# Kernel optimization log

Measured on AMD Instinct MI355X. Metric: run time of the kernel, lower is better.

The kernel has to match this reference:

```python
import jax, jax.numpy as jnp
import numpy as np

VOCAB, EMBED = 50000, 256
MODULES, HEADS, HID = 2, 4, 64
B, S = 8, 2048
LABELS = 16


def setup_inputs() -> dict:
    key = jax.random.key(0)
    ks = jax.random.split(key, 12)
    seqs = jax.random.randint(ks[0], (B, S), 0, VOCAB)
    emb = jax.random.normal(ks[1], (VOCAB, EMBED), jnp.float32) * 0.02
    Wq = jax.random.normal(ks[2], (MODULES, HEADS, HID, EMBED), jnp.float32) * (1.0 / np.sqrt(EMBED))
    bq = jax.random.normal(ks[3], (MODULES, HEADS, HID), jnp.float32) * 0.01
    Wk = jax.random.normal(ks[4], (MODULES, HEADS, HID, EMBED), jnp.float32) * (1.0 / np.sqrt(EMBED))
    bk = jax.random.normal(ks[5], (MODULES, HEADS, HID), jnp.float32) * 0.01
    Wv = jax.random.normal(ks[6], (MODULES, HEADS, HID, EMBED), jnp.float32) * (1.0 / np.sqrt(EMBED))
    bv = jax.random.normal(ks[7], (MODULES, HEADS, HID), jnp.float32) * 0.01
    Wz = jax.random.normal(ks[8], (MODULES, EMBED, HEADS * HID), jnp.float32) * (1.0 / np.sqrt(HEADS * HID))
    bz = jax.random.normal(ks[9], (MODULES, EMBED), jnp.float32) * 0.01
    Wo = jax.random.normal(ks[10], (LABELS, S * EMBED), jnp.float32) * (1.0 / np.sqrt(S * EMBED))
    bo = jax.random.normal(ks[11], (LABELS,), jnp.float32) * 0.01
    return {"seqs": seqs, "emb": emb, "Wq": Wq, "bq": bq, "Wk": Wk, "bk": bk,
            "Wv": Wv, "bv": bv, "Wz": Wz, "bz": bz, "Wo": Wo, "bo": bo}


def _forward(seqs, emb, Wq, bq, Wk, bk, Wv, bv, Wz, bz, Wo, bo):
    x = emb[seqs]  # [B, S, E]
    scale = jnp.float32(EMBED) ** 0.5
    for m in range(MODULES):
        # per-head projections with relu (dropout=0 / eval mode)
        Q = jax.nn.relu(jnp.einsum('bse,hde->bhsd', x, Wq[m]) + bq[m][None, :, None, :])
        K = jax.nn.relu(jnp.einsum('bse,hde->bhsd', x, Wk[m]) + bk[m][None, :, None, :])
        V = jax.nn.relu(jnp.einsum('bse,hde->bhsd', x, Wv[m]) + bv[m][None, :, None, :])
        QK = jnp.einsum('bhsd,bhtd->bhst', Q, K) / scale  # [B,H,S,S]
        # double softmax: first over the query axis (torch dim=1 of [B,S,S]),
        # then over the key axis (torch dim=2)
        A = jax.nn.softmax(QK, axis=2)
        A = jax.nn.softmax(A, axis=3)
        Z = jnp.einsum('bhst,bhtd->bhsd', A, V)  # [B,H,S,HID]
        Zall = jnp.transpose(Z, (0, 2, 1, 3)).reshape(x.shape[0], S, HEADS * HID)
        ZF = jnp.einsum('bsk,ek->bse', Zall, Wz[m]) + bz[m]
        x = ZF + x  # residual (layer_norm=False)
    Xf = x.reshape(x.shape[0], S * EMBED)
    y = jax.nn.sigmoid(Xf @ Wo.T + bo)
    return y


def reference(seqs, emb, Wq, bq, Wk, bk, Wv, bv, Wz, bz, Wo, bo):
    return _forward(seqs, emb, Wq, bq, Wk, bk, Wv, bv, Wz, bz, Wo, bo)
```

## Files before the change

### kernel.cpp

```cpp
#include <hip/hip_runtime.h>
#include <math.h>

#define Bb 8
#define Ss 2048
#define Ee 256
#define Hh 4
#define Dd 64

typedef unsigned short u16;
typedef unsigned int u32;
typedef __attribute__((ext_vector_type(8))) short bf16x8;
typedef __attribute__((ext_vector_type(4))) float f32x4;

__device__ __forceinline__ u16 f2bf(float f) {
  union { float f; u32 u; } c; c.f = f;
  return (u16)((c.u + 0x7FFFu + ((c.u >> 16) & 1u)) >> 16);
}
__device__ __forceinline__ float bf2f(u16 u) {
  union { u32 u; float f; } c; c.u = ((u32)u) << 16;
  return c.f;
}
__device__ __forceinline__ float bf2fs(short s) { return bf2f((u16)s); }

__global__ __launch_bounds__(256) void k_w2b(const float* __restrict__ src,
                                             u16* __restrict__ dst) {
  int idx = (blockIdx.x * 256 + threadIdx.x) * 4;
  float4 v = *reinterpret_cast<const float4*>(src + idx);
  ushort4 o;
  o.x = f2bf(v.x); o.y = f2bf(v.y); o.z = f2bf(v.z); o.w = f2bf(v.w);
  *reinterpret_cast<ushort4*>(dst + idx) = o;
}

__global__ __launch_bounds__(256) void k_gather(const int* __restrict__ seqs,
                                                const float* __restrict__ emb,
                                                float* __restrict__ x,
                                                u16* __restrict__ xb) {
  int idx = blockIdx.x * 256 + threadIdx.x;
  int row = idx >> 6, c4 = idx & 63;
  int tok = seqs[row];
  float4 v = reinterpret_cast<const float4*>(emb)[(size_t)tok * 64 + c4];
  reinterpret_cast<float4*>(x)[(size_t)row * 64 + c4] = v;
  ushort4 o;
  o.x = f2bf(v.x); o.y = f2bf(v.y); o.z = f2bf(v.z); o.w = f2bf(v.w);
  reinterpret_cast<ushort4*>(xb)[(size_t)row * 64 + c4] = o;
}

__global__ __launch_bounds__(256) void k_qkvm(const u16* __restrict__ xb,
    const u16* __restrict__ Wqb, const u16* __restrict__ Wkb, const u16* __restrict__ Wvb,
    const float* __restrict__ bq, const float* __restrict__ bk, const float* __restrict__ bv,
    u16* __restrict__ Qf, u16* __restrict__ Kf, u16* __restrict__ Vf, int mod) {
  __shared__ short Xs[128][72];
  __shared__ short Ws[128][72];
  int tid = threadIdx.x;
  int bn = blockIdx.x;
  int arr = bn >> 1, coff = (bn & 1) << 7;
  const u16* W = (arr == 0 ? Wqb : arr == 1 ? Wkb : Wvb) + (size_t)mod * 256 * 256;
  const float* bias = (arr == 0 ? bq : arr == 1 ? bk : bv) + mod * 256;
  u16* Out = (arr == 0 ? Qf : arr == 1 ? Kf : Vf);
  float oscale = (arr == 0) ? 0.0625f : 1.0f;
  int s0 = blockIdx.y * 128;
  int lr = tid >> 1, lc = (tid & 1) << 5;
  int w = tid >> 6, lane = tid & 63, ml = lane & 15, q = lane >> 4;
  int sh = (w >> 1) << 6, th = (w & 1) << 6;
  f32x4 acc[4][4] = {};
  for (int k0 = 0; k0 < 256; k0 += 64) {
#pragma unroll
    for (int hh = 0; hh < 4; hh++) {
      *reinterpret_cast<bf16x8*>(&Xs[lr][lc + hh * 8]) =
          *reinterpret_cast<const bf16x8*>(xb + (size_t)(s0 + lr) * Ee + k0 + lc + hh * 8);
      *reinterpret_cast<bf16x8*>(&Ws[lr][lc + hh * 8]) =
          *reinterpret_cast<const bf16x8*>(W + (size_t)(coff + lr) * Ee + k0 + lc + hh * 8);
    }
    __syncthreads();
#pragma unroll
    for (int ks = 0; ks < 2; ks++) {
      bf16x8 af[4], bfr[4];
#pragma unroll
      for (int mt = 0; mt < 4; mt++)
        af[mt] = *reinterpret_cast<const bf16x8*>(&Xs[sh + mt * 16 + ml][ks * 32 + q * 8]);
#pragma unroll
      for (int nt = 0; nt < 4; nt++)
        bfr[nt] = *reinterpret_cast<const bf16x8*>(&Ws[th + nt * 16 + ml][ks * 32 + q * 8]);
#pragma unroll
      for (int mt = 0; mt < 4; mt++)
#pragma unroll
        for (int nt = 0; nt < 4; nt++)
          acc[mt][nt] = __builtin_amdgcn_mfma_f32_16x16x32_bf16(af[mt], bfr[nt], acc[mt][nt], 0, 0, 0);
    }
    __syncthreads();
  }
#pragma unroll
  for (int mt = 0; mt < 4; mt++)
#pragma unroll
    for (int nt = 0; nt < 4; nt++)
#pragma unroll
      for (int r = 0; r < 4; r++) {
        int gm = s0 + sh + mt * 16 + q * 4 + r;
        int cc = coff + th + nt * 16 + ml;
        float v = acc[mt][nt][r] + bias[cc];
        v = (v > 0.f ? v : 0.f) * oscale;
        Out[(size_t)gm * Ee + cc] = f2bf(v);
      }
}

__global__ __launch_bounds__(256) void k_vt(const u16* __restrict__ Vf,
                                            u16* __restrict__ Vt) {
  __shared__ u16 T[64][72];
  int tid = threadIdx.x;
  int t0 = blockIdx.x * 64;
  int z = blockIdx.y;
  int b = z >> 2, h = z & 3;
  int lr = tid >> 2, lc = (tid & 3) << 4;
#pragma unroll
  for (int hh = 0; hh < 2; hh++) {
    bf16x8 v = *reinterpret_cast<const bf16x8*>(
        Vf + (size_t)(b * Ss + t0 + lr) * Ee + h * Dd + lc + hh * 8);
#pragma unroll
    for (int j = 0; j < 8; j++) T[lr][lc + hh * 8 + j] = (u16)v[j];
  }
  __syncthreads();
#pragma unroll
  for (int j = 0; j < 16; j++) {
    Vt[((size_t)z * Dd + lr) * Ss + t0 + lc + j] = T[lc + j][lr];
  }
}

__global__ __launch_bounds__(256) void k_vsum(const u16* __restrict__ Vt,
                                              float* __restrict__ SV) {
  int z = blockIdx.y;
  int d = blockIdx.x * 4 + (threadIdx.x >> 6);
  int lane = threadIdx.x & 63;
  const u16* row = Vt + ((size_t)z * Dd + d) * Ss;
  float s = 0.f;
#pragma unroll
  for (int it = 0; it < 4; it++) {
    bf16x8 v = *reinterpret_cast<const bf16x8*>(row + it * 512 + lane * 8);
#pragma unroll
    for (int j = 0; j < 8; j++) s += bf2fs(v[j]);
  }
#pragma unroll
  for (int off = 32; off; off >>= 1) s += __shfl_xor(s, off);
  if (lane == 0) SV[(size_t)z * Dd + d] = s;
}

__global__ __launch_bounds__(256) void k_csum(const u16* __restrict__ Qf,
    const u16* __restrict__ Kf, float* __restrict__ llic) {
  __shared__ short Qs[2][128 * 72];
  __shared__ float csm[4][64];
  int tid = threadIdx.x;
  int z = blockIdx.y, b = z >> 2, h = z & 3;
  const u16* Qb = Qf + (size_t)b * Ss * Ee + h * Dd;
  const u16* Kb = Kf + (size_t)b * Ss * Ee + h * Dd;
  int t0 = blockIdx.x * 128;
  int lr = tid >> 1, lc = (tid & 1) << 5;
  int w = tid >> 6, lane = tid & 63, ml = lane & 15, q = lane >> 4;
  int sh = (w >> 1) << 6, th = (w & 1) << 6;
  bf16x8 kb[2][4];
#pragma unroll
  for (int ks = 0; ks < 2; ks++)
#pragma unroll
    for (int nt = 0; nt < 4; nt++)
      kb[ks][nt] = *reinterpret_cast<const bf16x8*>(
          Kb + (size_t)(t0 + th + nt * 16 + ml) * Ee + ks * 32 + q * 8);
  float csum[4] = {};
  int p = 0;
  for (int s0 = 0; s0 < Ss; s0 += 128) {
#pragma unroll
    for (int hh = 0; hh < 4; hh++)
      *reinterpret_cast<bf16x8*>(&Qs[p][lr * 72 + lc + hh * 8]) =
          *reinterpret_cast<const bf16x8*>(Qb + (size_t)(s0 + lr) * Ee + lc + hh * 8);
    __syncthreads();
    f32x4 acc[4][4] = {};
#pragma unroll
    for (int ks = 0; ks < 2; ks++) {
      bf16x8 af[4];
#pragma unroll
      for (int mt = 0; mt < 4; mt++)
        af[mt] = *reinterpret_cast<const bf16x8*>(&Qs[p][(sh + mt * 16 + ml) * 72 + ks * 32 + q * 8]);
#pragma unroll
      for (int mt = 0; mt < 4; mt++)
#pragma unroll
        for (int nt = 0; nt < 4; nt++)
          acc[mt][nt] = __builtin_amdgcn_mfma_f32_16x16x32_bf16(af[mt], kb[ks][nt], acc[mt][nt], 0, 0, 0);
    }
#pragma unroll
    for (int nt = 0; nt < 4; nt++)
#pragma unroll
      for (int mt = 0; mt < 4; mt++)
#pragma unroll
        for (int r = 0; r < 4; r++)
          csum[nt] += __expf(acc[mt][nt][r]);
    p ^= 1;
  }
#pragma unroll
  for (int nt = 0; nt < 4; nt++) {
    csum[nt] += __shfl_xor(csum[nt], 16);
    csum[nt] += __shfl_xor(csum[nt], 32);
  }
  if (lane < 16) {
#pragma unroll
    for (int nt = 0; nt < 4; nt++) csm[w][nt * 16 + ml] = csum[nt];
  }
  __syncthreads();
  if (tid < 128) {
    int half = tid >> 6, c = tid & 63;
    float l = csm[half][c] + csm[half + 2][c];
    llic[(size_t)z * Ss + t0 + half * 64 + c] = -__logf(l);
  }
}

__global__ __launch_bounds__(256) void k_att(const u16* __restrict__ Qf,
    const u16* __restrict__ Kf, const u16* __restrict__ Vt,
    const float* __restrict__ llic, const float* __restrict__ SV,
    u16* __restrict__ Zb) {
  __shared__ short Ks[64 * 72];
  __shared__ short Vs[64 * 72];
  __shared__ short A2s[128 * 76];
  __shared__ float rs_s[2][128];
  int tid = threadIdx.x;
  int z = blockIdx.y, b = z >> 2, h = z & 3;
  const u16* Qb = Qf + (size_t)b * Ss * Ee + h * Dd;
  const u16* Kb = Kf + (size_t)b * Ss * Ee + h * Dd;
  const u16* VtZ = Vt + (size_t)z * Dd * Ss;
  const float* lz = llic + (size_t)z * Ss;
  int s0 = blockIdx.x * 128;
  int w = tid >> 6, lane = tid & 63, ml = lane & 15, q = lane >> 4;
  int wsd = (w >> 1) << 6, wt = (w & 1) << 5;
  bf16x8 qa[2][4];
#pragma unroll
  for (int ks = 0; ks < 2; ks++)
#pragma unroll
    for (int mt = 0; mt < 4; mt++)
      qa[ks][mt] = *reinterpret_cast<const bf16x8*>(
          Qb + (size_t)(s0 + wsd + mt * 16 + ml) * Ee + ks * 32 + q * 8);
  f32x4 acc2[2][4] = {};
  f32x4 rsv[4] = {};
  for (int t0 = 0; t0 < Ss; t0 += 64) {
    __syncthreads();
    if (tid < 128) {
      int r2 = tid >> 1, h2 = (tid & 1) << 5;
#pragma unroll
      for (int j = 0; j < 4; j++)
        *reinterpret_cast<bf16x8*>(&Ks[r2 * 72 + h2 + j * 8]) =
            *reinterpret_cast<const bf16x8*>(Kb + (size_t)(t0 + r2) * Ee + h2 + j * 8);
    } else {
      int t2 = tid - 128;
      int r2 = t2 >> 1, h2 = (t2 & 1) << 5;
#pragma unroll
      for (int j = 0; j < 4; j++)
        *reinterpret_cast<bf16x8*>(&Vs[r2 * 72 + h2 + j * 8]) =
            *reinterpret_cast<const bf16x8*>(VtZ + (size_t)r2 * Ss + t0 + h2 + j * 8);
    }
    __syncthreads();
    f32x4 acc[4][2] = {};
#pragma unroll
    for (int ks = 0; ks < 2; ks++) {
      bf16x8 bf[2];
#pragma unroll
      for (int nt = 0; nt < 2; nt++)
        bf[nt] = *reinterpret_cast<const bf16x8*>(&Ks[(wt + nt * 16 + ml) * 72 + ks * 32 + q * 8]);
#pragma unroll
      for (int mt = 0; mt < 4; mt++)
#pragma unroll
        for (int nt = 0; nt < 2; nt++)
          acc[mt][nt] = __builtin_amdgcn_mfma_f32_16x16x32_bf16(qa[ks][mt], bf[nt], acc[mt][nt], 0, 0, 0);
    }
#pragma unroll
    for (int nt = 0; nt < 2; nt++) {
      float lcv = lz[t0 + wt + nt * 16 + ml];
#pragma unroll
      for (int mt = 0; mt < 4; mt++)
#pragma unroll
        for (int r = 0; r < 4; r++) {
          float e1 = __expf(acc[mt][nt][r] + lcv);
          float p = e1 * (1.f + e1 * (0.5f + e1 * (0.166666667f + e1 * 0.0416666667f)));
          rsv[mt][r] += p;
          union { float f; u32 u; } cv; cv.f = p;
          A2s[(wsd + mt * 16 + q * 4 + r) * 76 + wt + nt * 16 + ml] =
              (short)((cv.u + 0x8000u) >> 16);
        }
    }
    __syncthreads();
#pragma unroll
    for (int ks = 0; ks < 2; ks++) {
      bf16x8 af2[2], bv[4];
#pragma unroll
      for (int mt2 = 0; mt2 < 2; mt2++)
        af2[mt2] = *reinterpret_cast<const bf16x8*>(&A2s[(w * 32 + mt2 * 16 + ml) * 76 + ks * 32 + q * 8]);
#pragma unroll
      for (int nt = 0; nt < 4; nt++)
        bv[nt] = *reinterpret_cast<const bf16x8*>(&Vs[(nt * 16 + ml) * 72 + ks * 32 + q * 8]);
#pragma unroll
      for (int mt2 = 0; mt2 < 2; mt2++)
#pragma unroll
        for (int nt = 0; nt < 4; nt++)
          acc2[mt2][nt] = __builtin_amdgcn_mfma_f32_16x16x32_bf16(af2[mt2], bv[nt], acc2[mt2][nt], 0, 0, 0);
    }
  }
#pragma unroll
  for (int mt = 0; mt < 4; mt++)
#pragma unroll
    for (int r = 0; r < 4; r++) {
      float v = rsv[mt][r];
      v += __shfl_xor(v, 1); v += __shfl_xor(v, 2);
      v += __shfl_xor(v, 4); v += __shfl_xor(v, 8);
      if (ml == 0) rs_s[w & 1][wsd + mt * 16 + q * 4 + r] = v;
    }
  __syncthreads();
  const float* SVz = SV + (size_t)z * Dd;
#pragma unroll
  for (int mt2 = 0; mt2 < 2; mt2++)
#pragma unroll
    for (int r = 0; r < 4; r++) {
      int row = w * 32 + mt2 * 16 + q * 4 + r;
      float inv = 1.f / (2048.f + rs_s[0][row] + rs_s[1][row]);
#pragma unroll
      for (int nt = 0; nt < 4; nt++) {
        float o = (SVz[nt * 16 + ml] + acc2[mt2][nt][r]) * inv;
        Zb[(size_t)(b * Ss + s0 + row) * Ee + h * Dd + nt * 16 + ml] = f2bf(o);
      }
    }
}

__global__ __launch_bounds__(256) void k_zfm(const u16* __restrict__ Zb,
    const u16* __restrict__ Wzb, const float* __restrict__ bzp,
    float* __restrict__ x, u16* __restrict__ xb, int mod) {
  __shared__ short Zs[128][72];
  __shared__ short Ws[128][72];
  int tid = threadIdx.x;
  int coff = blockIdx.x << 7;
  const u16* W = Wzb + (size_t)mod * 256 * 256;
  const float* bias = bzp + mod * Ee;
  int s0 = blockIdx.y * 128;
  int lr = tid >> 1, lc = (tid & 1) << 5;
  int w = tid >> 6, lane = tid & 63, ml = lane & 15, q = lane >> 4;
  int sh = (w >> 1) << 6, th = (w & 1) << 6;
  f32x4 acc[4][4] = {};
  for (int k0 = 0; k0 < 256; k0 += 64) {
#pragma unroll
    for (int hh = 0; hh < 4; hh++) {
      *reinterpret_cast<bf16x8*>(&Zs[lr][lc + hh * 8]) =
          *reinterpret_cast<const bf16x8*>(Zb + (size_t)(s0 + lr) * Ee + k0 + lc + hh * 8);
      *reinterpret_cast<bf16x8*>(&Ws[lr][lc + hh * 8]) =
          *reinterpret_cast<const bf16x8*>(W + (size_t)(coff + lr) * Ee + k0 + lc + hh * 8);
    }
    __syncthreads();
#pragma unroll
    for (int ks = 0; ks < 2; ks++) {
      bf16x8 af[4], bfr[4];
#pragma unroll
      for (int mt = 0; mt < 4; mt++)
        af[mt] = *reinterpret_cast<const bf16x8*>(&Zs[sh + mt * 16 + ml][ks * 32 + q * 8]);
#pragma unroll
      for (int nt = 0; nt < 4; nt++)
        bfr[nt] = *reinterpret_cast<const bf16x8*>(&Ws[th + nt * 16 + ml][ks * 32 + q * 8]);
#pragma unroll
      for (int mt = 0; mt < 4; mt++)
#pragma unroll
        for (int nt = 0; nt < 4; nt++)
          acc[mt][nt] = __builtin_amdgcn_mfma_f32_16x16x32_bf16(af[mt], bfr[nt], acc[mt][nt], 0, 0, 0);
    }
    __syncthreads();
  }
#pragma unroll
  for (int mt = 0; mt < 4; mt++)
#pragma unroll
    for (int nt = 0; nt < 4; nt++)
#pragma unroll
      for (int r = 0; r < 4; r++) {
        int gm = s0 + sh + mt * 16 + q * 4 + r;
        int gn = coff + th + nt * 16 + ml;
        float xv = x[(size_t)gm * Ee + gn] + acc[mt][nt][r] + bias[gn];
        x[(size_t)gm * Ee + gn] = xv;
        xb[(size_t)gm * Ee + gn] = f2bf(xv);
      }
}

__global__ __launch_bounds__(256) void k_final1(const float* __restrict__ x,
    const float* __restrict__ Wo, float* __restrict__ part) {
  int c = blockIdx.x, l = blockIdx.y, b = blockIdx.z;
  int tid = threadIdx.x;
  const float4* xr = reinterpret_cast<const float4*>(x + (size_t)b * (Ss * Ee) + c * 8192);
  const float4* wr = reinterpret_cast<const float4*>(Wo + (size_t)l * (Ss * Ee) + c * 8192);
  float sum = 0.f;
  for (int i = tid; i < 2048; i += 256) {
    float4 a = xr[i], w = wr[i];
    sum += a.x * w.x + a.y * w.y + a.z * w.z + a.w * w.w;
  }
  __shared__ float red[256];
  red[tid] = sum;
  __syncthreads();
  for (int o = 128; o; o >>= 1) {
    if (tid < o) red[tid] += red[tid + o];
    __syncthreads();
  }
  if (tid == 0) part[((b * 16 + l) << 6) + c] = red[0];
}

__global__ void k_final2(const float* __restrict__ part, const float* __restrict__ bo,
                         float* __restrict__ out) {
  int idx = threadIdx.x;
  int b = idx >> 4, l = idx & 15;
  float s = 0.f;
  for (int c = 0; c < 64; c++) s += part[((b * 16 + l) << 6) + c];
  s += bo[l];
  out[idx] = 1.f / (1.f + __expf(-s));
}

extern "C" void kernel_launch(void* const* d_in, const int* in_sizes, int n_in,
                              void* d_out, int out_size, void* d_ws, size_t ws_size,
                              hipStream_t stream) {
  const int*   seqs = (const int*)d_in[0];
  const float* emb  = (const float*)d_in[1];
  const float* Wq   = (const float*)d_in[2];
  const float* bq   = (const float*)d_in[3];
  const float* Wk   = (const float*)d_in[4];
  const float* bk   = (const float*)d_in[5];
  const float* Wv   = (const float*)d_in[6];
  const float* bv   = (const float*)d_in[7];
  const float* Wz   = (const float*)d_in[8];
  const float* bz   = (const float*)d_in[9];
  const float* Wo   = (const float*)d_in[10];
  const float* bo   = (const float*)d_in[11];
  float* out = (float*)d_out;
  float* ws  = (float*)d_ws;

  float* x    = ws;
  u16*   xb   = (u16*)(ws + 4194304);
  u16*   Qf   = (u16*)(ws + 6291456);
  u16*   Kf   = (u16*)(ws + 8388608);
  u16*   Vf   = (u16*)(ws + 10485760);
  u16*   Vt   = (u16*)(ws + 12582912);
  u16*   Zb   = (u16*)(ws + 14680064);
  float* SV   = ws + 16777216;
  float* part = ws + 16779264;
  u16*   Wqb  = (u16*)(ws + 16787456);
  u16*   Wkb  = (u16*)(ws + 16852992);
  u16*   Wvb  = (u16*)(ws + 16918528);
  u16*   Wzb  = (u16*)(ws + 16984064);
  float* llic = ws + 17049600;

  k_gather<<<(Bb * Ss * 64) / 256, 256, 0, stream>>>(seqs, emb, x, xb);
  k_w2b<<<131072 / 1024, 256, 0, stream>>>(Wq, Wqb);
  k_w2b<<<131072 / 1024, 256, 0, stream>>>(Wk, Wkb);
  k_w2b<<<131072 / 1024, 256, 0, stream>>>(Wv, Wvb);
  k_w2b<<<131072 / 1024, 256, 0, stream>>>(Wz, Wzb);

  for (int m = 0; m < 2; m++) {
    k_qkvm<<<dim3(6, 128), 256, 0, stream>>>(xb, Wqb, Wkb, Wvb, bq, bk, bv, Qf, Kf, Vf, m);
    k_vt<<<dim3(32, 32), 256, 0, stream>>>(Vf, Vt);
    k_vsum<<<dim3(16, 32), 256, 0, stream>>>(Vt, SV);
    k_csum<<<dim3(16, 32), 256, 0, stream>>>(Qf, Kf, llic);
    k_att<<<dim3(16, 32), 256, 0, stream>>>(Qf, Kf, Vt, llic, SV, Zb);
    k_zfm<<<dim3(2, 128), 256, 0, stream>>>(Zb, Wzb, bz, x, xb, m);
  }

  k_final1<<<dim3(64, 16, 8), 256, 0, stream>>>(x, Wo, part);
  k_final2<<<1, 128, 0, stream>>>(part, bo, out);
}
```

Baseline: 519.8 us.

## Halve attention tiles to 64 rows, double grid, and prefetch Q in csum

The column-sum and attention kernels now work on 64-row tiles instead of 128, and the grid doubles to 1024 blocks so the GPU has more blocks to spread across its compute units. Each wave owns one 16-row strip, so the cross-wave shared-memory reduction and one barrier per iteration in the attention kernel go away. The column-sum kernel now prefetches the next Q tile into the other buffer while computing on the current one. In exchange, K and V tiles are loaded from global memory twice as often in total, since each block reuses them across fewer rows.

```diff
diff --git a/kernel.cpp b/kernel.cpp
--- a/kernel.cpp
+++ b/kernel.cpp
@@ -145,181 +145,144 @@
 
 __global__ __launch_bounds__(256) void k_csum(const u16* __restrict__ Qf,
     const u16* __restrict__ Kf, float* __restrict__ llic) {
-  __shared__ short Qs[2][128 * 72];
-  __shared__ float csm[4][64];
+  __shared__ short Qs[2][128 * 68];
   int tid = threadIdx.x;
   int z = blockIdx.y, b = z >> 2, h = z & 3;
   const u16* Qb = Qf + (size_t)b * Ss * Ee + h * Dd;
   const u16* Kb = Kf + (size_t)b * Ss * Ee + h * Dd;
-  int t0 = blockIdx.x * 128;
+  int t0 = blockIdx.x * 64;
   int lr = tid >> 1, lc = (tid & 1) << 5;
   int w = tid >> 6, lane = tid & 63, ml = lane & 15, q = lane >> 4;
-  int sh = (w >> 1) << 6, th = (w & 1) << 6;
-  bf16x8 kb[2][4];
+  bf16x8 kb[2];
 #pragma unroll
   for (int ks = 0; ks < 2; ks++)
-#pragma unroll
-    for (int nt = 0; nt < 4; nt++)
-      kb[ks][nt] = *reinterpret_cast<const bf16x8*>(
-          Kb + (size_t)(t0 + th + nt * 16 + ml) * Ee + ks * 32 + q * 8);
-  float csum[4] = {};
-  int p = 0;
-  for (int s0 = 0; s0 < Ss; s0 += 128) {
-#pragma unroll
-    for (int hh = 0; hh < 4; hh++)
-      *reinterpret_cast<bf16x8*>(&Qs[p][lr * 72 + lc + hh * 8]) =
-          *reinterpret_cast<const bf16x8*>(Qb + (size_t)(s0 + lr) * Ee + lc + hh * 8);
-    __syncthreads();
-    f32x4 acc[4][4] = {};
-#pragma unroll
-    for (int ks = 0; ks < 2; ks++) {
-      bf16x8 af[4];
-#pragma unroll
-      for (int mt = 0; mt < 4; mt++)
-        af[mt] = *reinterpret_cast<const bf16x8*>(&Qs[p][(sh + mt * 16 + ml) * 72 + ks * 32 + q * 8]);
-#pragma unroll
-      for (int mt = 0; mt < 4; mt++)
-#pragma unroll
-        for (int nt = 0; nt < 4; nt++)
-          acc[mt][nt] = __builtin_amdgcn_mfma_f32_16x16x32_bf16(af[mt], kb[ks][nt], acc[mt][nt], 0, 0, 0);
-    }
-#pragma unroll
-    for (int nt = 0; nt < 4; nt++)
-#pragma unroll
-      for (int mt = 0; mt < 4; mt++)
-#pragma unroll
-        for (int r = 0; r < 4; r++)
-          csum[nt] += __expf(acc[mt][nt][r]);
-    p ^= 1;
-  }
-#pragma unroll
-  for (int nt = 0; nt < 4; nt++) {
-    csum[nt] += __shfl_xor(csum[nt], 16);
-    csum[nt] += __shfl_xor(csum[nt], 32);
-  }
-  if (lane < 16) {
-#pragma unroll
-    for (int nt = 0; nt < 4; nt++) csm[w][nt * 16 + ml] = csum[nt];
-  }
-  __syncthreads();
-  if (tid < 128) {
-    int half = tid >> 6, c = tid & 63;
-    float l = csm[half][c] + csm[half + 2][c];
-    llic[(size_t)z * Ss + t0 + half * 64 + c] = -__logf(l);
-  }
+    kb[ks] = *reinterpret_cast<const bf16x8*>(
+        Kb + (size_t)(t0 + w * 16 + ml) * Ee + ks * 32 + q * 8);
+#pragma unroll
+  for (int hh = 0; hh < 4; hh++)
+    *reinterpret_cast<bf16x8*>(&Qs[0][lr * 68 + lc + hh * 8]) =
+        *reinterpret_cast<const bf16x8*>(Qb + (size_t)lr * Ee + lc + hh * 8);
+  float csum = 0.f;
+  for (int i = 0; i < 16; i++) {
+    __syncthreads();
+    if (i + 1 < 16) {
+#pragma unroll
+      for (int hh = 0; hh < 4; hh++)
+        *reinterpret_cast<bf16x8*>(&Qs[(i + 1) & 1][lr * 68 + lc + hh * 8]) =
+            *reinterpret_cast<const bf16x8*>(
+                Qb + (size_t)((i + 1) * 128 + lr) * Ee + lc + hh * 8);
+    }
+    const short* Qcur = Qs[i & 1];
+#pragma unroll
+    for (int mt = 0; mt < 8; mt++) {
+      f32x4 acc = {};
+#pragma unroll
+      for (int ks = 0; ks < 2; ks++) {
+        bf16x8 af = *reinterpret_cast<const bf16x8*>(
+            &Qcur[(mt * 16 + ml) * 68 + ks * 32 + q * 8]);
+        acc = __builtin_amdgcn_mfma_f32_16x16x32_bf16(af, kb[ks], acc, 0, 0, 0);
+      }
+#pragma unroll
+      for (int r = 0; r < 4; r++) csum += __expf(acc[r]);
+    }
+  }
+  csum += __shfl_xor(csum, 16);
+  csum += __shfl_xor(csum, 32);
+  if (lane < 16)
+    llic[(size_t)z * Ss + t0 + w * 16 + ml] = -__logf(csum);
 }
 
 __global__ __launch_bounds__(256) void k_att(const u16* __restrict__ Qf,
     const u16* __restrict__ Kf, const u16* __restrict__ Vt,
     const float* __restrict__ llic, const float* __restrict__ SV,
     u16* __restrict__ Zb) {
-  __shared__ short Ks[64 * 72];
-  __shared__ short Vs[64 * 72];
-  __shared__ short A2s[128 * 76];
-  __shared__ float rs_s[2][128];
+  __shared__ short Ks[64 * 68];
+  __shared__ short Vs[64 * 68];
+  __shared__ short A2s[64 * 76];
   int tid = threadIdx.x;
   int z = blockIdx.y, b = z >> 2, h = z & 3;
   const u16* Qb = Qf + (size_t)b * Ss * Ee + h * Dd;
   const u16* Kb = Kf + (size_t)b * Ss * Ee + h * Dd;
   const u16* VtZ = Vt + (size_t)z * Dd * Ss;
   const float* lz = llic + (size_t)z * Ss;
-  int s0 = blockIdx.x * 128;
+  int s0 = blockIdx.x * 64;
   int w = tid >> 6, lane = tid & 63, ml = lane & 15, q = lane >> 4;
-  int wsd = (w >> 1) << 6, wt = (w & 1) << 5;
-  bf16x8 qa[2][4];
+  bf16x8 qa[2];
 #pragma unroll
   for (int ks = 0; ks < 2; ks++)
-#pragma unroll
-    for (int mt = 0; mt < 4; mt++)
-      qa[ks][mt] = *reinterpret_cast<const bf16x8*>(
-          Qb + (size_t)(s0 + wsd + mt * 16 + ml) * Ee + ks * 32 + q * 8);
-  f32x4 acc2[2][4] = {};
-  f32x4 rsv[4] = {};
+    qa[ks] = *reinterpret_cast<const bf16x8*>(
+        Qb + (size_t)(s0 + w * 16 + ml) * Ee + ks * 32 + q * 8);
+  f32x4 acc2[4] = {};
+  float rsv[4] = {};
   for (int t0 = 0; t0 < Ss; t0 += 64) {
     __syncthreads();
     if (tid < 128) {
       int r2 = tid >> 1, h2 = (tid & 1) << 5;
 #pragma unroll
       for (int j = 0; j < 4; j++)
-        *reinterpret_cast<bf16x8*>(&Ks[r2 * 72 + h2 + j * 8]) =
+        *reinterpret_cast<bf16x8*>(&Ks[r2 * 68 + h2 + j * 8]) =
             *reinterpret_cast<const bf16x8*>(Kb + (size_t)(t0 + r2) * Ee + h2 + j * 8);
     } else {
       int t2 = tid - 128;
       int r2 = t2 >> 1, h2 = (t2 & 1) << 5;
 #pragma unroll
       for (int j = 0; j < 4; j++)
-        *reinterpret_cast<bf16x8*>(&Vs[r2 * 72 + h2 + j * 8]) =
+        *reinterpret_cast<bf16x8*>(&Vs[r2 * 68 + h2 + j * 8]) =
             *reinterpret_cast<const bf16x8*>(VtZ + (size_t)r2 * Ss + t0 + h2 + j * 8);
     }
     __syncthreads();
-    f32x4 acc[4][2] = {};
+    f32x4 acc[4] = {};
 #pragma unroll
     for (int ks = 0; ks < 2; ks++) {
-      bf16x8 bf[2];
-#pragma unroll
-      for (int nt = 0; nt < 2; nt++)
-        bf[nt] = *reinterpret_cast<const bf16x8*>(&Ks[(wt + nt * 16 + ml) * 72 + ks * 32 + q * 8]);
-#pragma unroll
-      for (int mt = 0; mt < 4; mt++)
-#pragma unroll
-        for (int nt = 0; nt < 2; nt++)
-          acc[mt][nt] = __builtin_amdgcn_mfma_f32_16x16x32_bf16(qa[ks][mt], bf[nt], acc[mt][nt], 0, 0, 0);
-    }
-#pragma unroll
-    for (int nt = 0; nt < 2; nt++) {
-      float lcv = lz[t0 + wt + nt * 16 + ml];
-#pragma unroll
-      for (int mt = 0; mt < 4; mt++)
-#pragma unroll
-        for (int r = 0; r < 4; r++) {
-          float e1 = __expf(acc[mt][nt][r] + lcv);
-          float p = e1 * (1.f + e1 * (0.5f + e1 * (0.166666667f + e1 * 0.0416666667f)));
-          rsv[mt][r] += p;
-          union { float f; u32 u; } cv; cv.f = p;
-          A2s[(wsd + mt * 16 + q * 4 + r) * 76 + wt + nt * 16 + ml] =
-              (short)((cv.u + 0x8000u) >> 16);
-        }
-    }
-    __syncthreads();
+      bf16x8 bf[4];
+#pragma unroll
+      for (int nt = 0; nt < 4; nt++)
+        bf[nt] = *reinterpret_cast<const bf16x8*>(&Ks[(nt * 16 + ml) * 68 + ks * 32 + q * 8]);
+#pragma unroll
+      for (int nt = 0; nt < 4; nt++)
+        acc[nt] = __builtin_amdgcn_mfma_f32_16x16x32_bf16(qa[ks], bf[nt], acc[nt], 0, 0, 0);
+    }
+#pragma unroll
+    for (int nt = 0; nt < 4; nt++) {
+      float lcv = lz[t0 + nt * 16 + ml];
+#pragma unroll
+      for (int r = 0; r < 4; r++) {
+        float e1 = __expf(acc[nt][r] + lcv);
+        float p = e1 * (1.f + e1 * (0.5f + e1 * (0.166666667f + e1 * 0.0416666667f)));
+        rsv[r] += p;
+        union { float f; u32 u; } cv; cv.f = p;
+        A2s[(w * 16 + q * 4 + r) * 76 + nt * 16 + ml] = (short)((cv.u + 0x8000u) >> 16);
+      }
+    }
 #pragma unroll
     for (int ks = 0; ks < 2; ks++) {
-      bf16x8 af2[2], bv[4];
-#pragma unroll
-      for (int mt2 = 0; mt2 < 2; mt2++)
-        af2[mt2] = *reinterpret_cast<const bf16x8*>(&A2s[(w * 32 + mt2 * 16 + ml) * 76 + ks * 32 + q * 8]);
-#pragma unroll
-      for (int nt = 0; nt < 4; nt++)
-        bv[nt] = *reinterpret_cast<const bf16x8*>(&Vs[(nt * 16 + ml) * 72 + ks * 32 + q * 8]);
-#pragma unroll
-      for (int mt2 = 0; mt2 < 2; mt2++)
-#pragma unroll
-        for (int nt = 0; nt < 4; nt++)
-          acc2[mt2][nt] = __builtin_amdgcn_mfma_f32_16x16x32_bf16(af2[mt2], bv[nt], acc2[mt2][nt], 0, 0, 0);
-    }
-  }
-#pragma unroll
-  for (int mt = 0; mt < 4; mt++)
-#pragma unroll
-    for (int r = 0; r < 4; r++) {
-      float v = rsv[mt][r];
-      v += __shfl_xor(v, 1); v += __shfl_xor(v, 2);
-      v += __shfl_xor(v, 4); v += __shfl_xor(v, 8);
-      if (ml == 0) rs_s[w & 1][wsd + mt * 16 + q * 4 + r] = v;
-    }
-  __syncthreads();
+      bf16x8 af = *reinterpret_cast<const bf16x8*>(
+          &A2s[(w * 16 + ml) * 76 + ks * 32 + q * 8]);
+#pragma unroll
+      for (int nt = 0; nt < 4; nt++) {
+        bf16x8 bv = *reinterpret_cast<const bf16x8*>(&Vs[(nt * 16 + ml) * 68 + ks * 32 + q * 8]);
+        acc2[nt] = __builtin_amdgcn_mfma_f32_16x16x32_bf16(af, bv, acc2[nt], 0, 0, 0);
+      }
+    }
+  }
+#pragma unroll
+  for (int r = 0; r < 4; r++) {
+    float v = rsv[r];
+    v += __shfl_xor(v, 1); v += __shfl_xor(v, 2);
+    v += __shfl_xor(v, 4); v += __shfl_xor(v, 8);
+    rsv[r] = v;
+  }
   const float* SVz = SV + (size_t)z * Dd;
 #pragma unroll
-  for (int mt2 = 0; mt2 < 2; mt2++)
-#pragma unroll
-    for (int r = 0; r < 4; r++) {
-      int row = w * 32 + mt2 * 16 + q * 4 + r;
-      float inv = 1.f / (2048.f + rs_s[0][row] + rs_s[1][row]);
-#pragma unroll
-      for (int nt = 0; nt < 4; nt++) {
-        float o = (SVz[nt * 16 + ml] + acc2[mt2][nt][r]) * inv;
-        Zb[(size_t)(b * Ss + s0 + row) * Ee + h * Dd + nt * 16 + ml] = f2bf(o);
-      }
-    }
+  for (int r = 0; r < 4; r++) {
+    int row = s0 + w * 16 + q * 4 + r;
+    float inv = 1.f / (2048.f + rsv[r]);
+#pragma unroll
+    for (int nt = 0; nt < 4; nt++) {
+      float o = (SVz[nt * 16 + ml] + acc2[nt][r]) * inv;
+      Zb[(size_t)(b * Ss + row) * Ee + h * Dd + nt * 16 + ml] = f2bf(o);
+    }
+  }
 }
 
 __global__ __launch_bounds__(256) void k_zfm(const u16* __restrict__ Zb,
@@ -450,8 +413,8 @@
     k_qkvm<<<dim3(6, 128), 256, 0, stream>>>(xb, Wqb, Wkb, Wvb, bq, bk, bv, Qf, Kf, Vf, m);
     k_vt<<<dim3(32, 32), 256, 0, stream>>>(Vf, Vt);
     k_vsum<<<dim3(16, 32), 256, 0, stream>>>(Vt, SV);
-    k_csum<<<dim3(16, 32), 256, 0, stream>>>(Qf, Kf, llic);
-    k_att<<<dim3(16, 32), 256, 0, stream>>>(Qf, Kf, Vt, llic, SV, Zb);
+    k_csum<<<dim3(32, 32), 256, 0, stream>>>(Qf, Kf, llic);
+    k_att<<<dim3(32, 32), 256, 0, stream>>>(Qf, Kf, Vt, llic, SV, Zb);
     k_zfm<<<dim3(2, 128), 256, 0, stream>>>(Zb, Wzb, bz, x, xb, m);
   }
 
```

Result: slower. 676.2 us (+30.1%).
